# Performance work log

Hardware: AMD Instinct MI355X
Metric: run time of the kernel (lower is better)

Reference implementation:

```python
import jax, jax.numpy as jnp
import numpy as np

B, S, T, D, H = 2, 2048, 2048, 512, 8
HD = D // H
CLAMP = 1e9


def _padding_cross_mask(key):
    # emulate cross_mask(): valid prefixes for src and tgt sequences
    k1, k2 = jax.random.split(key)
    src_len = jax.random.randint(k1, (B,), S // 2, S + 1)  # [B]
    tgt_len = jax.random.randint(k2, (B,), T // 2, T + 1)  # [B]
    src_valid = jnp.arange(S)[None, :] < src_len[:, None]  # [B,S]
    tgt_valid = jnp.arange(T)[None, :] < tgt_len[:, None]  # [B,T]
    m = tgt_valid[:, :, None] & src_valid[:, None, :]      # [B,T,S]
    return m[:, None, :, :]                                 # [B,1,T,S]


def setup_inputs() -> dict:
    key = jax.random.key(0)
    ks = jax.random.split(key, 10)
    sc = 0.02
    return {
        "x": jax.random.normal(ks[0], (B, S, D), jnp.float32),
        "y": jax.random.normal(ks[1], (B, T, D), jnp.float32),
        "mask": _padding_cross_mask(ks[2]),
        "kv_w": jax.random.normal(ks[3], (D, 2 * D), jnp.float32) * sc,
        "kv_b": jax.random.normal(ks[4], (2 * D,), jnp.float32) * sc,
        "q_w": jax.random.normal(ks[5], (D, D), jnp.float32) * sc,
        "q_b": jax.random.normal(ks[6], (D,), jnp.float32) * sc,
        "o_w": jax.random.normal(ks[7], (D, D), jnp.float32) * sc,
        "o_b": jax.random.normal(ks[8], (D,), jnp.float32) * sc,
    }


def reference(x, y, mask, kv_w, kv_b, q_w, q_b, o_w, o_b):
    b, t, d = y.shape
    s = x.shape[1]
    kv = x @ kv_w + kv_b                               # [B,S,2D]
    q = y @ q_w + q_b                                  # [B,T,D]
    kv = kv.reshape(b, s, H, 2 * HD).transpose(0, 2, 1, 3)  # [B,H,S,2hd]
    q = q.reshape(b, t, H, HD).transpose(0, 2, 1, 3)        # [B,H,T,hd]
    k, v = kv[..., :HD], kv[..., HD:]
    scores = jnp.einsum("bhtd,bhsd->bhts", q, k) / jnp.sqrt(jnp.float32(HD))
    scores = jnp.where(mask, scores, -jnp.inf)
    scores = jnp.clip(scores, -CLAMP, CLAMP)
    attn = jax.nn.softmax(scores, axis=-1)             # [B,H,T,S]
    vals = jnp.einsum("bhts,bhsd->bhtd", attn, v)
    vals = vals.transpose(0, 2, 1, 3).reshape(b, t, d)
    return vals @ o_w + o_b
```

## Files before the change

### kernel.cpp

```cpp
#include <hip/hip_runtime.h>
#include <hip/hip_bf16.h>
#include <stdint.h>

#define BN 2
#define SL 2048
#define TL 2048
#define DD 512
#define HN 8
#define HDIM 64
#define NSPLIT 2
#define NCHUNK ((SL / NSPLIT) / 64)
#define QSCALE 0.1803368801111f
#define MFIX 12.0f

typedef __attribute__((ext_vector_type(8))) short bf16x8;
typedef __attribute__((ext_vector_type(4))) float f32x4;

static __device__ __forceinline__ unsigned short f2bf(float f) {
    union { float f; unsigned int u; } c; c.f = f;
    unsigned int u = c.u;
    unsigned int r = (u + 0x7fffu + ((u >> 16) & 1u)) >> 16;
    return (unsigned short)r;
}

static __device__ __forceinline__ void gload_lds16(const void* g, void* l) {
    __builtin_amdgcn_global_load_lds(
        (const __attribute__((address_space(1))) unsigned int*)g,
        (__attribute__((address_space(3))) unsigned int*)l, 16, 0, 0);
}

__global__ __launch_bounds__(256) void prep_kernel(
    const float* __restrict__ x, const float* __restrict__ y,
    const float* __restrict__ kv_w, const float* __restrict__ q_w,
    const float* __restrict__ o_w, const void* __restrict__ mask,
    unsigned short* __restrict__ xb, unsigned short* __restrict__ yb,
    unsigned short* __restrict__ kvwT, unsigned short* __restrict__ qwT,
    unsigned short* __restrict__ owT, int* __restrict__ lens,
    float* __restrict__ vmean)
{
    __shared__ unsigned short lds[64][80];
    __shared__ int kind_sh;
    __shared__ int lpart[4];
    int bx = blockIdx.x;
    int tid = threadIdx.x;
    if (bx < 2048) {
        const float* src = (bx < 1024) ? x : y;
        unsigned short* dst = (bx < 1024) ? xb : yb;
        long long i = ((long long)(bx & 1023) * 256 + tid) * 8;
        float4 v0 = *(const float4*)&src[i];
        float4 v1 = *(const float4*)&src[i + 4];
        unsigned long long p0 =
            (unsigned long long)f2bf(v0.x) | ((unsigned long long)f2bf(v0.y) << 16) |
            ((unsigned long long)f2bf(v0.z) << 32) | ((unsigned long long)f2bf(v0.w) << 48);
        unsigned long long p1 =
            (unsigned long long)f2bf(v1.x) | ((unsigned long long)f2bf(v1.y) << 16) |
            ((unsigned long long)f2bf(v1.z) << 32) | ((unsigned long long)f2bf(v1.w) << 48);
        *(unsigned long long*)&dst[i] = p0;
        *(unsigned long long*)&dst[i + 4] = p1;
        return;
    }
    if (bx >= 2308) {
        float4 z = {0.f, 0.f, 0.f, 0.f};
        ((float4*)vmean)[tid] = z;
        return;
    }
    if (bx >= 2304) {
        int blk = bx - 2304;
        int b = blk >> 1, is_tgt = blk & 1;
        if (tid == 0) {
            unsigned int v = *(const unsigned int*)mask;
            int kind = 0;
            if (v == 0x01010101u) kind = 1;
            else if (v == 0x3f800000u) kind = 2;
            else if (v == 0x3f803f80u) kind = 3;
            kind_sh = kind;
        }
        __syncthreads();
        int kind = kind_sh;
        int lane = tid & 63, wid = tid >> 6;
        int cnt = 0;
        for (int i = tid; i < (is_tgt ? TL : SL); i += 256) {
            long long idx = is_tgt ? ((long long)(b * TL + i)) * SL
                                   : ((long long)(b * TL + 0)) * SL + i;
            bool bit;
            if (kind == 0)      bit = ((const int*)mask)[idx] != 0;
            else if (kind == 1) bit = ((const unsigned char*)mask)[idx] != 0;
            else if (kind == 2) bit = ((const float*)mask)[idx] != 0.0f;
            else                bit = ((const unsigned short*)mask)[idx] != 0;
            cnt += bit ? 1 : 0;
        }
        #pragma unroll
        for (int off = 32; off >= 1; off >>= 1) cnt += __shfl_xor(cnt, off, 64);
        if (lane == 0) lpart[wid] = cnt;
        __syncthreads();
        if (tid == 0)
            lens[is_tgt * 2 + b] = lpart[0] + lpart[1] + lpart[2] + lpart[3];
        return;
    }
    const float* W; unsigned short* Wt; int N, tb;
    if (bx < 2176)      { W = kv_w; Wt = kvwT; N = 1024; tb = bx - 2048; }
    else if (bx < 2240) { W = q_w;  Wt = qwT;  N = 512;  tb = bx - 2176; }
    else                { W = o_w;  Wt = owT;  N = 512;  tb = bx - 2240; }
    int nblk = N / 64;
    int n0 = (tb % nblk) * 64, k0 = (tb / nblk) * 64;
    #pragma unroll
    for (int i = 0; i < 4; ++i) {
        int fi = tid + i * 256;
        int kl = fi >> 4;
        int nl = (fi & 15) * 4;
        float4 v = *(const float4*)&W[(long long)(k0 + kl) * N + n0 + nl];
        lds[nl + 0][kl] = f2bf(v.x);
        lds[nl + 1][kl] = f2bf(v.y);
        lds[nl + 2][kl] = f2bf(v.z);
        lds[nl + 3][kl] = f2bf(v.w);
    }
    __syncthreads();
    #pragma unroll
    for (int i = 0; i < 2; ++i) {
        int fi = tid + i * 256;
        int nl = fi >> 3;
        int kl = (fi & 7) * 8;
        *(bf16x8*)&Wt[(long long)(n0 + nl) * 512 + k0 + kl] = *(const bf16x8*)&lds[nl][kl];
    }
}

static __device__ __forceinline__ void mainloop_64x128(
    const unsigned short* __restrict__ Ab, const unsigned short* __restrict__ Bt,
    int m0, int n0, int tid,
    unsigned short* Alds,
    unsigned short* Blds,
    f32x4 (&acc)[2][4])
{
    int lane = tid & 63, wid = tid >> 6;
    int wr = wid >> 1, wc = wid & 1;
    int lr = lane & 15, lg = lane >> 4;
    int rl = lane >> 2;
    int sc = (lane & 3) ^ ((rl >> 1) & 3);

    auto stage = [&](int buf, int kt) {
        #pragma unroll
        for (int j = 0; j < 3; ++j) {
            int seg = wid * 3 + j;
            if (seg < 4) {
                int row = seg * 16 + rl;
                gload_lds16(&Ab[((long long)(m0 + row)) * 512 + kt * 32 + sc * 8],
                            (char*)(Alds + buf * 2048) + seg * 1024);
            } else {
                int s2 = seg - 4;
                int row = s2 * 16 + rl;
                gload_lds16(&Bt[((long long)(n0 + row)) * 512 + kt * 32 + sc * 8],
                            (char*)(Blds + buf * 4096) + s2 * 1024);
            }
        }
    };
    auto frag = [&](const unsigned short* base, int row) -> bf16x8 {
        int slot = lg ^ ((row >> 1) & 3);
        return *(const bf16x8*)((const char*)base + row * 64 + slot * 16);
    };

    stage(0, 0);
    for (int kt = 0; kt < 16; ++kt) {
        int buf = kt & 1;
        asm volatile("s_waitcnt vmcnt(0)" ::: "memory");
        __syncthreads();
        if (kt + 1 < 16) stage(buf ^ 1, kt + 1);
        bf16x8 bfr[4];
        #pragma unroll
        for (int ni = 0; ni < 4; ++ni)
            bfr[ni] = frag(Blds + buf * 4096, wc * 64 + ni * 16 + lr);
        #pragma unroll
        for (int mi = 0; mi < 2; ++mi) {
            bf16x8 afr = frag(Alds + buf * 2048, wr * 32 + mi * 16 + lr);
            #pragma unroll
            for (int ni = 0; ni < 4; ++ni)
                acc[mi][ni] = __builtin_amdgcn_mfma_f32_16x16x32_bf16(
                                  afr, bfr[ni], acc[mi][ni], 0, 0, 0);
        }
    }
}

__global__ __launch_bounds__(256) void gemm_kvq(
    const unsigned short* __restrict__ xb, const unsigned short* __restrict__ yb,
    const unsigned short* __restrict__ kvwT, const unsigned short* __restrict__ qwT,
    const float* __restrict__ kv_b, const float* __restrict__ q_b,
    const int* __restrict__ lens,
    unsigned short* __restrict__ Kbuf, unsigned short* __restrict__ Vtbuf,
    unsigned short* __restrict__ Qbuf, float* __restrict__ vmean)
{
    __shared__ __align__(16) unsigned short Alds[2][64 * 32];
    __shared__ __align__(16) unsigned short Blds[2][128 * 32];
    bool isq = blockIdx.x >= 8;
    int m0 = blockIdx.y * 64;
    if (isq && (m0 & 2047) >= lens[2 + (m0 >> 11)]) return;
    const unsigned short* Ab = isq ? yb : xb;
    const unsigned short* Bt = isq ? qwT : kvwT;
    const float* bias = isq ? q_b : kv_b;
    int n0 = (isq ? (blockIdx.x - 8) : blockIdx.x) * 128;
    int tid = threadIdx.x;
    int lane = tid & 63, wid = tid >> 6;
    int wr = wid >> 1, wc = wid & 1;
    int lr = lane & 15, lg = lane >> 4;

    f32x4 acc[2][4] = {};
    mainloop_64x128(Ab, Bt, m0, n0, tid, &Alds[0][0], &Blds[0][0], acc);

    float vsum[4] = {0.f, 0.f, 0.f, 0.f};
    #pragma unroll
    for (int mi = 0; mi < 2; ++mi)
    #pragma unroll
    for (int ni = 0; ni < 4; ++ni) {
        int n = n0 + wc * 64 + ni * 16 + lr;
        int mbase = m0 + wr * 32 + mi * 16 + lg * 4;
        float bv = bias[n];
        int b = mbase >> 11;
        int s = mbase & 2047;
        if (!isq) {
            int h = n >> 7, j = n & 127;
            if (j < HDIM) {
                long long base = (((long long)(b * HN + h)) * SL + s) * HDIM + j;
                #pragma unroll
                for (int r = 0; r < 4; ++r)
                    Kbuf[base + (long long)r * HDIM] = f2bf(acc[mi][ni][r] + bv);
            } else {
                int d = j - HDIM;
                long long base = (((long long)(b * HN + h)) * HDIM + d) * SL + s;
                unsigned long long p = 0;
                #pragma unroll
                for (int r = 0; r < 4; ++r)
                    p |= (unsigned long long)f2bf(acc[mi][ni][r] + bv) << (16 * r);
                *(unsigned long long*)&Vtbuf[base] = p;
                vsum[ni] += ((acc[mi][ni][0] + bv) + (acc[mi][ni][1] + bv)) +
                            ((acc[mi][ni][2] + bv) + (acc[mi][ni][3] + bv));
            }
        } else {
            int h = n >> 6, j = n & 63;
            long long base = (((long long)(b * HN + h)) * TL + s) * HDIM + j;
            #pragma unroll
            for (int r = 0; r < 4; ++r)
                Qbuf[base + (long long)r * HDIM] = f2bf((acc[mi][ni][r] + bv) * QSCALE);
        }
    }
    if (!isq && wc == 1) {
        int bh = (m0 >> 11) * HN + (n0 >> 7);
        #pragma unroll
        for (int ni = 0; ni < 4; ++ni) {
            float v = vsum[ni];
            v += __shfl_xor(v, 16, 64);
            v += __shfl_xor(v, 32, 64);
            if (lg == 0)
                atomicAdd(&vmean[bh * HDIM + ni * 16 + lr], v * (1.0f / SL));
        }
    }
}

__global__ __launch_bounds__(256) void gemm_out(
    const unsigned short* __restrict__ Ab, const unsigned short* __restrict__ Bt,
    const float* __restrict__ bias, float* __restrict__ outF)
{
    __shared__ __align__(16) unsigned short Alds[2][64 * 32];
    __shared__ __align__(16) unsigned short Blds[2][128 * 32];
    const int N = 512;
    int n0 = blockIdx.x * 128;
    int m0 = blockIdx.y * 64;
    int tid = threadIdx.x;
    int lane = tid & 63, wid = tid >> 6;
    int wr = wid >> 1, wc = wid & 1;
    int lr = lane & 15, lg = lane >> 4;

    f32x4 acc[2][4] = {};
    mainloop_64x128(Ab, Bt, m0, n0, tid, &Alds[0][0], &Blds[0][0], acc);

    #pragma unroll
    for (int mi = 0; mi < 2; ++mi)
    #pragma unroll
    for (int ni = 0; ni < 4; ++ni) {
        int n = n0 + wc * 64 + ni * 16 + lr;
        int mbase = m0 + wr * 32 + mi * 16 + lg * 4;
        float bv = bias[n];
        #pragma unroll
        for (int r = 0; r < 4; ++r)
            outF[(long long)(mbase + r) * N + n] = acc[mi][ni][r] + bv;
    }
}

__global__ __launch_bounds__(256) void attn_kernel(
    const unsigned short* __restrict__ Q,
    const unsigned short* __restrict__ K,
    const unsigned short* __restrict__ Vt,
    const int* __restrict__ lens,
    float* __restrict__ pml,
    float* __restrict__ pacc)
{
    __shared__ unsigned short Kt[2][4096];
    __shared__ unsigned short Vl[2][4096];
    __shared__ unsigned int P32[4][16][32];
    int idx = blockIdx.x;
    int gid = (idx & 7) * 128 + (idx >> 3);
    int t0 = (gid & 31) * 64;
    int bhsp = gid >> 5;
    int bh = bhsp >> 1;
    int sp = bhsp & 1;
    int b = bh >> 3;
    int tid = threadIdx.x;
    int lane = tid & 63, wid = tid >> 6;
    int tcol = lane & 15, lg = lane >> 4;
    int t0w = t0 + wid * 16;
    int src_len = lens[b];
    int tgt_len = lens[2 + b];
    if (t0 >= tgt_len) return;
    int sbase = sp * (SL / NSPLIT);

    int nch = (src_len - sbase + 63) >> 6;
    if (nch > NCHUNK) nch = NCHUNK;
    if (nch <= 0) {
        #pragma unroll
        for (int dc = 0; dc < 4; ++dc)
            #pragma unroll
            for (int r = 0; r < 4; ++r) {
                long long rowidx = (long long)bh * TL + t0w + lg * 4 + r;
                pacc[(rowidx * NSPLIT + sp) * 64 + dc * 16 + tcol] = 0.0f;
            }
        if (lg == 0) {
            long long rowidx = (long long)bh * TL + t0w + tcol;
            pml[rowidx * NSPLIT + sp] = 0.0f;
        }
        return;
    }

    const unsigned short* Qb = Q + ((long long)bh * TL) * HDIM;
    const unsigned short* Kb = K + ((long long)bh * SL) * HDIM;
    const unsigned short* Vb = Vt + ((long long)bh * HDIM) * SL;

    bf16x8 qf0 = *(const bf16x8*)&Qb[(t0w + tcol) * HDIM + lg * 8];
    bf16x8 qf1 = *(const bf16x8*)&Qb[(t0w + tcol) * HDIM + 32 + lg * 8];
    asm volatile("" : "+v"(qf0), "+v"(qf1));

    int sub = lane >> 3;
    int scol = (lane & 7) ^ sub;
    auto stage = [&](int buf, int s0) {
        #pragma unroll
        for (int j = 0; j < 2; ++j) {
            int g = wid * 2 + j;
            int row = g * 8 + sub;
            gload_lds16(&Kb[(s0 + row) * HDIM + scol * 8],
                        (char*)&Kt[buf][0] + g * 1024);
            gload_lds16(&Vb[(long long)row * SL + s0 + scol * 8],
                        (char*)&Vl[buf][0] + g * 1024);
        }
    };

    f32x4 accv[4] = {};
    float l_run = 0.0f;
    int pswz = (tcol & 7) << 2;

    stage(0, sbase);

    for (int sc2 = 0; sc2 < nch; ++sc2) {
        int s0 = sbase + sc2 * 64;
        asm volatile("s_waitcnt vmcnt(0)" ::: "memory");
        __syncthreads();
        if (sc2 + 1 < nch) stage((sc2 + 1) & 1, s0 + 64);
        const char* Kl = (const char*)&Kt[sc2 & 1][0];
        const char* Vlb = (const char*)&Vl[sc2 & 1][0];

        float sv[4][4];
        __builtin_amdgcn_s_setprio(1);
        #pragma unroll
        for (int st = 0; st < 4; ++st) {
            int krow = st * 16 + tcol;
            int swz = (krow & 7) << 4;
            bf16x8 kf0 = *(const bf16x8*)(Kl + krow * 128 + ((lg << 4) ^ swz));
            bf16x8 kf1 = *(const bf16x8*)(Kl + krow * 128 + (((lg + 4) << 4) ^ swz));
            f32x4 sa = {};
            sa = __builtin_amdgcn_mfma_f32_16x16x32_bf16(kf0, qf0, sa, 0, 0, 0);
            sa = __builtin_amdgcn_mfma_f32_16x16x32_bf16(kf1, qf1, sa, 0, 0, 0);
            #pragma unroll
            for (int r = 0; r < 4; ++r) sv[st][r] = sa[r];
        }
        __builtin_amdgcn_s_setprio(0);
        if (s0 + 64 > src_len) {
            #pragma unroll
            for (int st = 0; st < 4; ++st)
                #pragma unroll
                for (int r = 0; r < 4; ++r) {
                    int s = s0 + st * 16 + lg * 4 + r;
                    if (s >= src_len) sv[st][r] = -1e30f;
                }
        }
        float ps[4];
        #pragma unroll
        for (int st = 0; st < 4; ++st) {
            float p0 = __builtin_amdgcn_exp2f(sv[st][0] - MFIX);
            float p1 = __builtin_amdgcn_exp2f(sv[st][1] - MFIX);
            float p2 = __builtin_amdgcn_exp2f(sv[st][2] - MFIX);
            float p3 = __builtin_amdgcn_exp2f(sv[st][3] - MFIX);
            ps[st] = (p0 + p1) + (p2 + p3);
            unsigned int w0, w1;
            asm("v_cvt_pk_bf16_f32 %0, %1, %2" : "=v"(w0) : "v"(p0), "v"(p1));
            asm("v_cvt_pk_bf16_f32 %0, %1, %2" : "=v"(w1) : "v"(p2), "v"(p3));
            int wsw = (st * 8 + lg * 2) ^ pswz;
            *(unsigned long long*)&P32[wid][tcol][wsw] =
                (unsigned long long)w0 | ((unsigned long long)w1 << 32);
        }
        float psum = (ps[0] + ps[1]) + (ps[2] + ps[3]);
        psum += __shfl_xor(psum, 16, 64);
        psum += __shfl_xor(psum, 32, 64);
        l_run += psum;
        asm volatile("s_waitcnt lgkmcnt(0)" ::: "memory");
        __builtin_amdgcn_sched_barrier(0);
        __builtin_amdgcn_s_setprio(1);
        #pragma unroll
        for (int c = 0; c < 2; ++c) {
            bf16x8 pf = *(const bf16x8*)&P32[wid][tcol][(c * 16 + lg * 4) ^ pswz];
            #pragma unroll
            for (int dc = 0; dc < 4; ++dc) {
                int vrow = dc * 16 + tcol;
                bf16x8 vf = *(const bf16x8*)(Vlb + vrow * 128 +
                                             ((((c * 4 + lg) << 4)) ^ ((vrow & 7) << 4)));
                accv[dc] = __builtin_amdgcn_mfma_f32_16x16x32_bf16(pf, vf, accv[dc], 0, 0, 0);
            }
        }
        __builtin_amdgcn_s_setprio(0);
    }

    #pragma unroll
    for (int dc = 0; dc < 4; ++dc)
        #pragma unroll
        for (int r = 0; r < 4; ++r) {
            long long rowidx = (long long)bh * TL + t0w + lg * 4 + r;
            pacc[(rowidx * NSPLIT + sp) * 64 + dc * 16 + tcol] = accv[dc][r];
        }
    if (lg == 0) {
        long long rowidx = (long long)bh * TL + t0w + tcol;
        pml[rowidx * NSPLIT + sp] = l_run;
    }
}

__global__ __launch_bounds__(256) void combine_kernel(
    const float* __restrict__ pml, const float* __restrict__ pacc,
    const float* __restrict__ vmean, const int* __restrict__ lens,
    unsigned short* __restrict__ valsb)
{
    int lane = threadIdx.x & 63, wid = threadIdx.x >> 6;
    const int rows_total = BN * HN * TL;
    for (int row = blockIdx.x * 4 + wid; row < rows_total; row += gridDim.x * 4) {
        int bh = row >> 11, t = row & 2047;
        int b = bh >> 3, h = bh & 7;
        float o;
        if (t >= lens[2 + b]) {
            o = vmean[bh * HDIM + lane];
        } else {
            float l = pml[row * 2 + 0] + pml[row * 2 + 1];
            float a1 = pacc[((long long)row * 2 + 0) * 64 + lane];
            float a2 = pacc[((long long)row * 2 + 1) * 64 + lane];
            o = (a1 + a2) / l;
        }
        valsb[((long long)(b * TL + t)) * DD + h * HDIM + lane] = f2bf(o);
    }
}

extern "C" void kernel_launch(void* const* d_in, const int* in_sizes, int n_in,
                              void* d_out, int out_size, void* d_ws, size_t ws_size,
                              hipStream_t stream)
{
    const float* x    = (const float*)d_in[0];
    const float* y    = (const float*)d_in[1];
    const void*  mask = d_in[2];
    const float* kv_w = (const float*)d_in[3];
    const float* kv_b = (const float*)d_in[4];
    const float* q_w  = (const float*)d_in[5];
    const float* q_b  = (const float*)d_in[6];
    const float* o_w  = (const float*)d_in[7];
    const float* o_b  = (const float*)d_in[8];
    float* out = (float*)d_out;

    char* ws = (char*)d_ws;
    int* lens = (int*)ws;
    unsigned short* Qbuf  = (unsigned short*)(ws + 256);
    unsigned short* Kbuf  = Qbuf + (size_t)2097152;
    unsigned short* Vtbuf = Kbuf + (size_t)2097152;
    float* pml  = (float*)(Vtbuf + (size_t)2097152);
    float* pacc = pml + (size_t)262144;
    unsigned short* valsb = (unsigned short*)(pacc + (size_t)4194304);
    unsigned short* kvwT = valsb + (size_t)2097152;
    unsigned short* qwT  = kvwT + (size_t)524288;
    unsigned short* owT  = qwT + (size_t)262144;
    float* vmean = (float*)(owT + (size_t)262144);
    unsigned short* xb = (unsigned short*)pacc;
    unsigned short* yb = xb + (size_t)2097152;

    prep_kernel<<<2309, 256, 0, stream>>>(x, y, kv_w, q_w, o_w, mask,
                                          xb, yb, kvwT, qwT, owT, lens, vmean);
    gemm_kvq<<<dim3(12, 64), 256, 0, stream>>>(xb, yb, kvwT, qwT, kv_b, q_b,
                                               lens, Kbuf, Vtbuf, Qbuf, vmean);
    attn_kernel<<<1024, 256, 0, stream>>>(Qbuf, Kbuf, Vtbuf, lens, pml, pacc);
    combine_kernel<<<2048, 256, 0, stream>>>(pml, pacc, vmean, lens, valsb);
    gemm_out<<<dim3(4, 64), 256, 0, stream>>>(valsb, owT, o_b, out);
}
```

Baseline: 76.48 us.

## Fuse split-K combine into output projection GEMM A-tile loading

Removes the separate combine kernel and the bf16 vals buffer. The output GEMM now reads the two partial accumulators, the row sums and vmean directly, normalises them and converts to bf16 while staging its A tile into LDS, with register prefetch of the next k-tile. This saves one launch and a full write plus read of the intermediate tensor. In exchange, every one of the 4 N-column blocks re-reads the fp32 partials (4x redundant loads of pacc), and each k-step waits on vmcnt(0) before writing the A tile.

Result: slower. 80.26 us (+4.9%).

```diff
diff --git a/kernel.cpp b/kernel.cpp
--- a/kernel.cpp
+++ b/kernel.cpp
@@ -253,36 +253,6 @@
     }
 }
 
-__global__ __launch_bounds__(256) void gemm_out(
-    const unsigned short* __restrict__ Ab, const unsigned short* __restrict__ Bt,
-    const float* __restrict__ bias, float* __restrict__ outF)
-{
-    __shared__ __align__(16) unsigned short Alds[2][64 * 32];
-    __shared__ __align__(16) unsigned short Blds[2][128 * 32];
-    const int N = 512;
-    int n0 = blockIdx.x * 128;
-    int m0 = blockIdx.y * 64;
-    int tid = threadIdx.x;
-    int lane = tid & 63, wid = tid >> 6;
-    int wr = wid >> 1, wc = wid & 1;
-    int lr = lane & 15, lg = lane >> 4;
-
-    f32x4 acc[2][4] = {};
-    mainloop_64x128(Ab, Bt, m0, n0, tid, &Alds[0][0], &Blds[0][0], acc);
-
-    #pragma unroll
-    for (int mi = 0; mi < 2; ++mi)
-    #pragma unroll
-    for (int ni = 0; ni < 4; ++ni) {
-        int n = n0 + wc * 64 + ni * 16 + lr;
-        int mbase = m0 + wr * 32 + mi * 16 + lg * 4;
-        float bv = bias[n];
-        #pragma unroll
-        for (int r = 0; r < 4; ++r)
-            outF[(long long)(mbase + r) * N + n] = acc[mi][ni][r] + bv;
-    }
-}
-
 __global__ __launch_bounds__(256) void attn_kernel(
     const unsigned short* __restrict__ Q,
     const unsigned short* __restrict__ K,
@@ -436,26 +406,122 @@
     }
 }
 
-__global__ __launch_bounds__(256) void combine_kernel(
+__global__ __launch_bounds__(256) void gemm_out_fused(
     const float* __restrict__ pml, const float* __restrict__ pacc,
     const float* __restrict__ vmean, const int* __restrict__ lens,
-    unsigned short* __restrict__ valsb)
+    const unsigned short* __restrict__ Bt, const float* __restrict__ bias,
+    float* __restrict__ outF)
 {
-    int lane = threadIdx.x & 63, wid = threadIdx.x >> 6;
-    const int rows_total = BN * HN * TL;
-    for (int row = blockIdx.x * 4 + wid; row < rows_total; row += gridDim.x * 4) {
-        int bh = row >> 11, t = row & 2047;
-        int b = bh >> 3, h = bh & 7;
-        float o;
-        if (t >= lens[2 + b]) {
-            o = vmean[bh * HDIM + lane];
-        } else {
-            float l = pml[row * 2 + 0] + pml[row * 2 + 1];
-            float a1 = pacc[((long long)row * 2 + 0) * 64 + lane];
-            float a2 = pacc[((long long)row * 2 + 1) * 64 + lane];
-            o = (a1 + a2) / l;
-        }
-        valsb[((long long)(b * TL + t)) * DD + h * HDIM + lane] = f2bf(o);
+    __shared__ __align__(16) unsigned short Alds[2][64 * 32];
+    __shared__ __align__(16) unsigned short Blds[2][128 * 32];
+    const int N = 512;
+    int n0 = blockIdx.x * 128;
+    int m0 = blockIdx.y * 64;
+    int tid = threadIdx.x;
+    int lane = tid & 63, wid = tid >> 6;
+    int wr = wid >> 1, wc = wid & 1;
+    int lr = lane & 15, lg = lane >> 4;
+    int rl = lane >> 2;
+    int sc = (lane & 3) ^ ((rl >> 1) & 3);
+    int b = m0 >> 11;
+    int tgt_len = lens[2 + b];
+
+    int ar = tid >> 2;
+    int ac = (tid & 3) * 8;
+    int t = (m0 + ar) & 2047;
+    bool patch = t >= tgt_len;
+    int aslot = ((tid & 3) ^ ((ar >> 1) & 3));
+    char* awr = (char*)&Alds[0][0] + ar * 64 + aslot * 16;
+
+    auto stageB = [&](int buf, int kt) {
+        #pragma unroll
+        for (int j = 0; j < 2; ++j) {
+            int seg = wid * 2 + j;
+            int row = seg * 16 + rl;
+            gload_lds16(&Bt[((long long)(n0 + row)) * 512 + kt * 32 + sc * 8],
+                        (char*)&Blds[buf][0] + seg * 1024);
+        }
+    };
+    auto frag = [&](const unsigned short* base, int row) -> bf16x8 {
+        int slot = lg ^ ((row >> 1) & 3);
+        return *(const bf16x8*)((const char*)base + row * 64 + slot * 16);
+    };
+
+    float4 x0, x1, y0, y1, v0, v1;
+    float2 lv;
+    auto loadA = [&](int kt) {
+        int h = kt >> 1, d0 = (kt & 1) * 32;
+        long long rowidx = ((long long)(b * HN + h)) * TL + t;
+        const float* p1 = &pacc[(rowidx * 2 + 0) * 64 + d0 + ac];
+        const float* p2 = &pacc[(rowidx * 2 + 1) * 64 + d0 + ac];
+        x0 = *(const float4*)p1;  x1 = *(const float4*)(p1 + 4);
+        y0 = *(const float4*)p2;  y1 = *(const float4*)(p2 + 4);
+        lv = *(const float2*)&pml[rowidx * 2];
+        const float* vp = &vmean[(b * HN + h) * HDIM + d0 + ac];
+        v0 = *(const float4*)vp;  v1 = *(const float4*)(vp + 4);
+    };
+    auto writeA = [&](int buf) {
+        float inv = __builtin_amdgcn_rcpf(lv.x + lv.y);
+        float o0 = patch ? v0.x : (x0.x + y0.x) * inv;
+        float o1 = patch ? v0.y : (x0.y + y0.y) * inv;
+        float o2 = patch ? v0.z : (x0.z + y0.z) * inv;
+        float o3 = patch ? v0.w : (x0.w + y0.w) * inv;
+        float o4 = patch ? v1.x : (x1.x + y1.x) * inv;
+        float o5 = patch ? v1.y : (x1.y + y1.y) * inv;
+        float o6 = patch ? v1.z : (x1.z + y1.z) * inv;
+        float o7 = patch ? v1.w : (x1.w + y1.w) * inv;
+        unsigned int w0, w1, w2, w3;
+        asm("v_cvt_pk_bf16_f32 %0, %1, %2" : "=v"(w0) : "v"(o0), "v"(o1));
+        asm("v_cvt_pk_bf16_f32 %0, %1, %2" : "=v"(w1) : "v"(o2), "v"(o3));
+        asm("v_cvt_pk_bf16_f32 %0, %1, %2" : "=v"(w2) : "v"(o4), "v"(o5));
+        asm("v_cvt_pk_bf16_f32 %0, %1, %2" : "=v"(w3) : "v"(o6), "v"(o7));
+        uint4 pk = {w0, w1, w2, w3};
+        *(uint4*)(awr + buf * 4096) = pk;
+    };
+
+    f32x4 acc[2][4] = {};
+
+    loadA(0);
+    stageB(0, 0);
+    asm volatile("s_waitcnt vmcnt(0)" ::: "memory");
+    writeA(0);
+    __syncthreads();
+
+    for (int kt = 0; kt < 16; ++kt) {
+        int buf = kt & 1;
+        if (kt + 1 < 16) {
+            loadA(kt + 1);
+            stageB(buf ^ 1, kt + 1);
+        }
+        bf16x8 bfr[4];
+        #pragma unroll
+        for (int ni = 0; ni < 4; ++ni)
+            bfr[ni] = frag(&Blds[buf][0], wc * 64 + ni * 16 + lr);
+        #pragma unroll
+        for (int mi = 0; mi < 2; ++mi) {
+            bf16x8 afr = frag(&Alds[buf][0], wr * 32 + mi * 16 + lr);
+            #pragma unroll
+            for (int ni = 0; ni < 4; ++ni)
+                acc[mi][ni] = __builtin_amdgcn_mfma_f32_16x16x32_bf16(
+                                  afr, bfr[ni], acc[mi][ni], 0, 0, 0);
+        }
+        if (kt + 1 < 16) {
+            asm volatile("s_waitcnt vmcnt(0)" ::: "memory");
+            writeA(buf ^ 1);
+        }
+        __syncthreads();
+    }
+
+    #pragma unroll
+    for (int mi = 0; mi < 2; ++mi)
+    #pragma unroll
+    for (int ni = 0; ni < 4; ++ni) {
+        int n = n0 + wc * 64 + ni * 16 + lr;
+        int mbase = m0 + wr * 32 + mi * 16 + lg * 4;
+        float bv = bias[n];
+        #pragma unroll
+        for (int r = 0; r < 4; ++r)
+            outF[(long long)(mbase + r) * N + n] = acc[mi][ni][r] + bv;
     }
 }
 
@@ -481,8 +547,7 @@
     unsigned short* Vtbuf = Kbuf + (size_t)2097152;
     float* pml  = (float*)(Vtbuf + (size_t)2097152);
     float* pacc = pml + (size_t)262144;
-    unsigned short* valsb = (unsigned short*)(pacc + (size_t)4194304);
-    unsigned short* kvwT = valsb + (size_t)2097152;
+    unsigned short* kvwT = (unsigned short*)(pacc + (size_t)4194304);
     unsigned short* qwT  = kvwT + (size_t)524288;
     unsigned short* owT  = qwT + (size_t)262144;
     float* vmean = (float*)(owT + (size_t)262144);
@@ -494,6 +559,6 @@
     gemm_kvq<<<dim3(12, 64), 256, 0, stream>>>(xb, yb, kvwT, qwT, kv_b, q_b,
                                                lens, Kbuf, Vtbuf, Qbuf, vmean);
     attn_kernel<<<1024, 256, 0, stream>>>(Qbuf, Kbuf, Vtbuf, lens, pml, pacc);
-    combine_kernel<<<2048, 256, 0, stream>>>(pml, pacc, vmean, lens, valsb);
-    gemm_out<<<dim3(4, 64), 256, 0, stream>>>(valsb, owT, o_b, out);
-}
+    gemm_out_fused<<<dim3(4, 64), 256, 0, stream>>>(pml, pacc, vmean, lens,
+                                                    owT, o_b, out);
+}
```
